# Kernel tuning notes

Measured on AMD Instinct MI355X. Metric: run time of the kernel, lower is better.

Reference implementation:

```python
import jax, jax.numpy as jnp
import numpy as np
import math

N_HEADS = 8
EPS = 1e-12


def _ln(x, g, b):
    m = x.mean(-1, keepdims=True)
    v = ((x - m) ** 2).mean(-1, keepdims=True)
    return (x - m) * jax.lax.rsqrt(v + EPS) * g + b


def _ffn(x, w1, b1, w2, b2):
    # torch nn.GELU default = exact erf gelu; dropout is identity in eval
    return jax.nn.gelu(x @ w1 + b1, approximate=False) @ w2 + b2


def _mha(q_in, kv, mask, qw, qb, kw, kb, vw, vb, ow, ob):
    B, S, _ = q_in.shape
    dh = qw.shape[1] // N_HEADS

    def split(x):
        return x.reshape(B, S, N_HEADS, dh).transpose(0, 2, 1, 3)  # (B,H,S,dh)

    q = split(q_in @ qw + qb) / math.sqrt(dh)
    k = split(kv @ kw + kb)
    v = split(kv @ vw + vb)
    scores = jnp.einsum('bhqd,bhkd->bhqk', q, k) + mask[:, None]
    w = jax.nn.softmax(scores, axis=-1)
    ctx = jnp.einsum('bhqk,bhkd->bhqd', w, v)
    ctx = ctx.transpose(0, 2, 1, 3).reshape(B, S, N_HEADS * dh)
    return ctx @ ow + ob


def reference(hidden, lens,
              f_ffn_w1, f_ffn_b1, f_ffn_w2, f_ffn_b2, f_ln_g, f_ln_b,
              f_q_w, f_q_b, f_k_w, f_k_b, f_v_w, f_v_b, f_o_w, f_o_b,
              b_ffn_w1, b_ffn_b1, b_ffn_w2, b_ffn_b2, b_ln_g, b_ln_b,
              b_q_w, b_q_b, b_k_w, b_k_b, b_v_w, b_v_b, b_o_w, b_o_b,
              attn_ln_g, attn_ln_b,
              out_ffn_w1, out_ffn_b1, out_ffn_w2, out_ffn_b2,
              out_ln_g, out_ln_b):
    S, B, D2 = hidden.shape
    H = D2 // 2
    S2 = S - 2
    f = hidden[..., :H]
    bk = hidden[..., H:]
    query = jnp.concatenate([f[:-2], bk[2:]], axis=-1)        # (S2, B, 2H)
    qbf = jnp.swapaxes(query, 0, 1)                            # (B, S2, 2H)

    # vectorized per-sample length-dependent masks (additive, 0 / -inf)
    qi = jnp.arange(S2)[:, None]
    ki = jnp.arange(S2)[None, :]
    Lm = (lens - 2)[:, None, None]
    # forward: rows >= L-2 all zero; valid rows causal (k <= q) inside [0, L-2)
    f_mask = jnp.where((qi >= Lm) | (ki <= qi), 0.0, -np.inf).astype(hidden.dtype)
    # backward: rows >= L-2 all zero; valid rows anti-causal (k >= q) with k < L-2
    b_mask = jnp.where((qi >= Lm) | ((ki >= qi) & (ki < Lm)), 0.0, -np.inf).astype(hidden.dtype)

    f_q = _ln(_ffn(qbf, f_ffn_w1, f_ffn_b1, f_ffn_w2, f_ffn_b2), f_ln_g, f_ln_b)
    f_kv = jnp.swapaxes(f[:-2], 0, 1)
    f_attn = _mha(f_q, f_kv, f_mask, f_q_w, f_q_b, f_k_w, f_k_b, f_v_w, f_v_b, f_o_w, f_o_b)

    b_q = _ln(_ffn(qbf, b_ffn_w1, b_ffn_b1, b_ffn_w2, b_ffn_b2), b_ln_g, b_ln_b)
    b_kv = jnp.swapaxes(bk[2:], 0, 1)
    b_attn = _mha(b_q, b_kv, b_mask, b_q_w, b_q_b, b_k_w, b_k_b, b_v_w, b_v_b, b_o_w, b_o_b)

    attn_out = _ln(qbf + jnp.concatenate([f_attn, b_attn], axis=-1), attn_ln_g, attn_ln_b)
    out = _ln(_ffn(attn_out, out_ffn_w1, out_ffn_b1, out_ffn_w2, out_ffn_b2), out_ln_g, out_ln_b)
    return jnp.swapaxes(out, 0, 1)                             # (S2, B, 2H)


def setup_inputs():
    key = jax.random.key(0)
    ks = jax.random.split(key, 16)
    S, B, H = 1024, 8, 512
    d = {}
    d['hidden'] = jax.random.normal(ks[0], (S, B, 2 * H), jnp.float32)
    d['lens'] = jax.random.randint(ks[1], (B,), 4, S + 1)

    def w(k, i, o):
        return jax.random.normal(k, (i, o), jnp.float32) * 0.02

    idx = 2
    for p in ('f', 'b'):
        d[p + '_ffn_w1'] = w(ks[idx], 2 * H, 2 * H); idx += 1
        d[p + '_ffn_b1'] = jnp.zeros((2 * H,), jnp.float32)
        d[p + '_ffn_w2'] = w(ks[idx], 2 * H, H); idx += 1
        d[p + '_ffn_b2'] = jnp.zeros((H,), jnp.float32)
        d[p + '_ln_g'] = jnp.ones((H,), jnp.float32)
        d[p + '_ln_b'] = jnp.zeros((H,), jnp.float32)
        for n in ('q', 'k', 'v', 'o'):
            d[p + '_' + n + '_w'] = w(jax.random.fold_in(ks[idx], hash(n) % 97), H, H)
            d[p + '_' + n + '_b'] = jnp.zeros((H,), jnp.float32)
        idx += 1
    d['attn_ln_g'] = jnp.ones((2 * H,), jnp.float32)
    d['attn_ln_b'] = jnp.zeros((2 * H,), jnp.float32)
    d['out_ffn_w1'] = w(ks[idx], 2 * H, 2 * H); idx += 1
    d['out_ffn_b1'] = jnp.zeros((2 * H,), jnp.float32)
    d['out_ffn_w2'] = w(ks[idx], 2 * H, 2 * H); idx += 1
    d['out_ffn_b2'] = jnp.zeros((2 * H,), jnp.float32)
    d['out_ln_g'] = jnp.ones((2 * H,), jnp.float32)
    d['out_ln_b'] = jnp.zeros((2 * H,), jnp.float32)
    return d
```

## Files before the change

kernel.cpp:

```cpp
#include <hip/hip_runtime.h>
#include <cmath>

#define S_ 1024
#define B_ 8
#define H_ 512
#define S2_ 1022
#define M_ (B_*S2_)
#define PAD_ 8192
#define VTS_ ((size_t)8*8*64*1024)

typedef __attribute__((ext_vector_type(8))) short bf16x8;
typedef __attribute__((ext_vector_type(4))) float f32x4;
typedef __attribute__((ext_vector_type(4))) unsigned int u32x4;
typedef __attribute__((ext_vector_type(2))) unsigned int u32x2;

__device__ __forceinline__ unsigned short f2bf(float f){
  unsigned int u = __float_as_uint(f);
  return (unsigned short)((u + 0x7fffu + ((u>>16)&1u)) >> 16);
}
__device__ __forceinline__ float bf2f(unsigned short u){
  return __uint_as_float((unsigned int)u << 16);
}
__device__ __forceinline__ float fgelu(float x){
  float u = x * (0.7978845608f + 0.0356774081f * x * x);
// ... 153 lines not shown
          else {
            int sr = row % S2_, bb2 = row / S2_;
            ((float*)Cout)[((size_t)sr * B_ + bb2) * ldc + col0 + f*16] = v;
          }
        }
      }
    }
  }
}

__global__ __launch_bounds__(512, 2) void lma_gemm8(
    const unsigned short* __restrict__ A, int lda,
    const unsigned short* __restrict__ Bt0, const unsigned short* __restrict__ Bt1,
    const float* __restrict__ bias0, const float* __restrict__ bias1,
    unsigned short* __restrict__ Cout, int ldc,
    int M, int N, int K, int mode, int amap, int nmt)
{
  __shared__ unsigned short Ls[2][2][256*64];
  const int tid = threadIdx.x;
  const int w = tid >> 6, lane = tid & 63, quad = lane >> 4, l16 = lane & 15;
  const int mt = blockIdx.x % nmt, nt = blockIdx.x / nmt;
  const int m0 = mt * 256, n0 = nt * 256;
  const int brch = m0 >> 13;
  const unsigned short* Bt = brch ? Bt1 : Bt0;
  const float* bias = brch ? bias1 : bias0;
  const int coloff = (amap == 2 && brch) ? 512 : 0;
  const int wm = (w >> 2) * 128, wn = (w & 3) * 64;

  f32x4 acc[8][4];
  #pragma unroll
  for (int i = 0; i < 8; i++)
    #pragma unroll
    for (int f = 0; f < 4; f++) acc[i][f] = f32x4{0.f,0.f,0.f,0.f};

  const int lrow8 = lane >> 3;
  const int lkb   = lane & 7;
  const int NT = K >> 6;

  const unsigned short* aP[2][2]; const unsigned short* bP[2][2];
  int aD[2][2], bD[2][2];
  #pragma unroll
  for (int hf = 0; hf < 2; hf++)
    #pragma unroll
    for (int c = 0; c < 2; c++) {
      int rtA = (w>>2)*128 + hf*64 + ((w&3)*2 + c)*8 + lrow8;
      int kbA = lkb ^ (rtA & 7);
      int ga = m0 + rtA;
      int ar;
      if (amap == 0) { ar = (ga > M-1) ? (M-1) : ga; }
      else { ar = ga & (PAD_-1); if (ar > M_-1) ar = M_-1; }
      aP[hf][c] = A + (size_t)ar * lda + coloff + kbA*8;
      aD[hf][c] = ((w>>2)*128 + hf*64 + ((w&3)*2 + c)*8) * 64;
      int rtB = (w>>1)*64 + hf*32 + ((w&1)*2 + c)*8 + lrow8;
      int kbB = lkb ^ (rtB & 7);
      int gb = n0 + rtB; if (gb > N-1) gb = N-1;
      bP[hf][c] = Bt + (size_t)gb * K + kbB*8;
      bD[hf][c] = ((w>>1)*64 + hf*32 + ((w&1)*2 + c)*8) * 64;
    }

  bf16x8 af[4][2], bf[2][2];

  #define STA(buf, hf, kt) { _Pragma("unroll") for (int c = 0; c < 2; c++) \
      glds16(aP[hf][c] + (size_t)(kt)*64, &Ls[buf][0][aD[hf][c]]); }
  #define STB(buf, hf, kt) { _Pragma("unroll") for (int c = 0; c < 2; c++) \
      glds16(bP[hf][c] + (size_t)(kt)*64, &Ls[buf][1][bD[hf][c]]); }
  #define LDA8(buf, mq) { _Pragma("unroll") for (int j = 0; j < 4; j++){ \
      int rt = wm + (mq)*64 + j*16 + l16; \
      const unsigned short* base = &Ls[buf][0][rt*64]; \
      int f_ = rt & 7; \
      af[j][0] = *(const bf16x8*)(base + ((    quad) ^ f_)*8); \
      af[j][1] = *(const bf16x8*)(base + ((4 + quad) ^ f_)*8); } }
  #define LDB8(buf, nq) { _Pragma("unroll") for (int j = 0; j < 2; j++){ \
      int rt = wn + (nq)*32 + j*16 + l16; \
      const unsigned short* base = &Ls[buf][1][rt*64]; \
      int f_ = rt & 7; \
      bf[j][0] = *(const bf16x8*)(base + ((    quad) ^ f_)*8); \
      bf[j][1] = *(const bf16x8*)(base + ((4 + quad) ^ f_)*8); } }
  #define MFMAQ(mq, nq) { __builtin_amdgcn_s_setprio(1); \
      _Pragma("unroll") for (int j = 0; j < 4; j++) \
        _Pragma("unroll") for (int j2 = 0; j2 < 2; j2++){ \
          acc[(mq)*4+j][(nq)*2+j2] = __builtin_amdgcn_mfma_f32_16x16x32_bf16(af[j][0], bf[j2][0], acc[(mq)*4+j][(nq)*2+j2], 0, 0, 0); \
          acc[(mq)*4+j][(nq)*2+j2] = __builtin_amdgcn_mfma_f32_16x16x32_bf16(af[j][1], bf[j2][1], acc[(mq)*4+j][(nq)*2+j2], 0, 0, 0); } \
      __builtin_amdgcn_s_setprio(0); }
  #define BAR()   { SB(); __builtin_amdgcn_s_barrier(); SB(); }
  #define LGKM0() { asm volatile("s_waitcnt lgkmcnt(0)" ::: "memory"); SB(); }
  #define VM6()   { asm volatile("s_waitcnt vmcnt(6)"   ::: "memory"); SB(); }
  #define VM2()   { asm volatile("s_waitcnt vmcnt(2)"   ::: "memory"); SB(); }

  STA(0, 0, 0); STB(0, 0, 0); STB(0, 1, 0); STA(0, 1, 0);
  STA(1, 0, 1);
  asm volatile("s_waitcnt vmcnt(2)" ::: "memory"); SB();
  BAR();

  const int NI = NT >> 1;
  for (int i = 0; i < NI; i++) {
    const int tb  = 2*i + 1;
    int ta2 = 2*i + 2; if (ta2 > NT-1) ta2 = NT-1;
    int tb2 = 2*i + 3; if (tb2 > NT-1) tb2 = NT-1;

    LDA8(0, 0); LDB8(0, 0); STB(1, 0, tb);
    BAR(); LGKM0(); MFMAQ(0, 0); BAR();
    LDB8(0, 1); STB(1, 1, tb);
    BAR(); LGKM0(); MFMAQ(0, 1); BAR();
    LDA8(0, 1); STA(1, 1, tb);
    BAR(); LGKM0(); MFMAQ(1, 1); BAR();
    LDB8(0, 0); STA(0, 0, ta2);
    BAR(); LGKM0(); MFMAQ(1, 0); VM6(); BAR();
    LDA8(1, 0); LDB8(1, 0); STB(0, 1, ta2);
    BAR(); LGKM0(); MFMAQ(0, 0); VM6(); BAR();
    LDB8(1, 1); STA(0, 1, ta2);
    BAR(); LGKM0(); MFMAQ(0, 1); VM6(); BAR();
    LDA8(1, 1); STB(0, 0, ta2);
    BAR(); LGKM0(); MFMAQ(1, 1); BAR();
    LDB8(1, 0); STA(1, 0, tb2);
    BAR(); LGKM0(); MFMAQ(1, 0); VM2(); BAR();
  }
  asm volatile("s_waitcnt vmcnt(0)" ::: "memory");

  float bv[4];
  #pragma unroll
  for (int f = 0; f < 4; f++) bv[f] = bias ? bias[n0 + wn + f*16 + l16] : 0.f;
  const int col0 = n0 + wn + l16;
  #pragma unroll
  for (int i2 = 0; i2 < 8; i2++) {
    #pragma unroll
    for (int r = 0; r < 4; r++) {
      int row = m0 + wm + i2*16 + quad*4 + r;
      if (row < M) {
        #pragma unroll
        for (int f = 0; f < 4; f++) {
          float v = acc[i2][f][r] + bv[f];
          if (mode == 2) v = fgelu(v);
          Cout[(size_t)row * ldc + col0 + f*16] = f2bf(v);
        }
      }
    }
  }
  #undef STA
  #undef STB
  #undef LDA8
  #undef LDB8
  #undef MFMAQ
  #undef BAR
  #undef LGKM0
  #undef VM6
  #undef VM2
}

__global__ __launch_bounds__(512, 2) void lma_gemm8w(
    const unsigned short* __restrict__ A, int lda,
    const unsigned short* __restrict__ Bt0, const unsigned short* __restrict__ Bt1,
    const float* __restrict__ bias0, const float* __restrict__ bias1,
    void* __restrict__ Cout, int ldc,
    int M, int N, int K, int mode, int nmt)
{
  __shared__ unsigned short LsA[2][128*64];
  __shared__ unsigned short LsB[2][256*64];
  const int tid = threadIdx.x;
  const int w = tid >> 6, lane = tid & 63, quad = lane >> 4, l16 = lane & 15;
  const int mt = blockIdx.x % nmt, nt = blockIdx.x / nmt;
  const int m0 = mt * 128, n0 = nt * 256;
  const int brch = m0 >> 13;
  const unsigned short* Bt = brch ? Bt1 : Bt0;
  const float* bias = brch ? bias1 : bias0;
  const int wm = (w >> 2) * 64, wn = (w & 3) * 64;

  f32x4 acc[4][4];
  #pragma unroll
  for (int i = 0; i < 4; i++)
    #pragma unroll
    for (int f = 0; f < 4; f++) acc[i][f] = f32x4{0.f,0.f,0.f,0.f};

  const int lrow8 = lane >> 3;
  const int lkb   = lane & 7;
  const int NT = K >> 6;

  const unsigned short* aP[2]; int aD[2];
  const unsigned short* bP[2][2]; int bD[2][2];
  #pragma unroll
  for (int hf = 0; hf < 2; hf++) {
    int rtA = hf*64 + w*8 + lrow8;
    int kbA = lkb ^ (rtA & 7);
    int ga = m0 + rtA; if (ga > M-1) ga = M-1;
    aP[hf] = A + (size_t)ga * lda + kbA*8;
    aD[hf] = (hf*64 + w*8) * 64;
    #pragma unroll
    for (int c = 0; c < 2; c++) {
      int rtB = hf*128 + (w*2 + c)*8 + lrow8;
      int kbB = lkb ^ (rtB & 7);
      int gb = n0 + rtB; if (gb > N-1) gb = N-1;
      bP[hf][c] = Bt + (size_t)gb * K + kbB*8;
      bD[hf][c] = (hf*128 + (w*2 + c)*8) * 64;
    }
  }

  bf16x8 af[2][2], bf[2][2];

  #define WSTA(buf, hf, kt) { glds16(aP[hf] + (size_t)(kt)*64, &LsA[buf][aD[hf]]); }
  #define WSTB(buf, hf, kt) { _Pragma("unroll") for (int c = 0; c < 2; c++) \
      glds16(bP[hf][c] + (size_t)(kt)*64, &LsB[buf][bD[hf][c]]); }
  #define WLDA(buf, mq) { _Pragma("unroll") for (int j = 0; j < 2; j++){ \
      int rt = wm + (mq)*32 + j*16 + l16; \
      const unsigned short* base = &LsA[buf][rt*64]; \
      int f_ = rt & 7; \
      af[j][0] = *(const bf16x8*)(base + ((    quad) ^ f_)*8); \
      af[j][1] = *(const bf16x8*)(base + ((4 + quad) ^ f_)*8); } }
  #define WLDB(buf, nq) { _Pragma("unroll") for (int j = 0; j < 2; j++){ \
      int rt = wn + (nq)*32 + j*16 + l16; \
      const unsigned short* base = &LsB[buf][rt*64]; \
      int f_ = rt & 7; \
      bf[j][0] = *(const bf16x8*)(base + ((    quad) ^ f_)*8); \
      bf[j][1] = *(const bf16x8*)(base + ((4 + quad) ^ f_)*8); } }
  #define WMFMAQ(mq, nq) { __builtin_amdgcn_s_setprio(1); \
      _Pragma("unroll") for (int j = 0; j < 2; j++) \
        _Pragma("unroll") for (int j2 = 0; j2 < 2; j2++){ \
          acc[(mq)*2+j][(nq)*2+j2] = __builtin_amdgcn_mfma_f32_16x16x32_bf16(af[j][0], bf[j2][0], acc[(mq)*2+j][(nq)*2+j2], 0, 0, 0); \
          acc[(mq)*2+j][(nq)*2+j2] = __builtin_amdgcn_mfma_f32_16x16x32_bf16(af[j][1], bf[j2][1], acc[(mq)*2+j][(nq)*2+j2], 0, 0, 0); } \
      __builtin_amdgcn_s_setprio(0); }
  #define WBAR()   { SB(); __builtin_amdgcn_s_barrier(); SB(); }
  #define WLGKM0() { asm volatile("s_waitcnt lgkmcnt(0)" ::: "memory"); SB(); }
  #define WVM4()   { asm volatile("s_waitcnt vmcnt(4)"   ::: "memory"); SB(); }
  #define WVM1()   { asm volatile("s_waitcnt vmcnt(1)"   ::: "memory"); SB(); }

  WSTA(0, 0, 0); WSTB(0, 0, 0); WSTB(0, 1, 0); WSTA(0, 1, 0);
  WSTA(1, 0, 1);
  WVM1(); WBAR();

  const int NI = NT >> 1;
  for (int i = 0; i < NI; i++) {
    const int tb  = 2*i + 1;
    int ta2 = 2*i + 2; if (ta2 > NT-1) ta2 = NT-1;
    int tb2 = 2*i + 3; if (tb2 > NT-1) tb2 = NT-1;

    WLDA(0, 0); WLDB(0, 0); WSTB(1, 0, tb);
    WBAR(); WLGKM0(); WMFMAQ(0, 0); WBAR();
    WLDB(0, 1); WSTB(1, 1, tb);
    WBAR(); WLGKM0(); WMFMAQ(0, 1); WBAR();
    WLDA(0, 1); WSTA(1, 1, tb);
    WBAR(); WLGKM0(); WMFMAQ(1, 1); WBAR();
    WLDB(0, 0); WSTA(0, 0, ta2);
    WBAR(); WLGKM0(); WMFMAQ(1, 0); WVM4(); WBAR();
    WLDA(1, 0); WLDB(1, 0); WSTB(0, 1, ta2);
    WBAR(); WLGKM0(); WMFMAQ(0, 0); WVM4(); WBAR();
    WLDB(1, 1); WSTA(0, 1, ta2);
    WBAR(); WLGKM0(); WMFMAQ(0, 1); WVM4(); WBAR();
    WLDA(1, 1); WSTB(0, 0, ta2);
    WBAR(); WLGKM0(); WMFMAQ(1, 1); WBAR();
    WLDB(1, 0); WSTA(1, 0, tb2);
    WBAR(); WLGKM0(); WMFMAQ(1, 0); WVM1(); WBAR();
  }
  asm volatile("s_waitcnt vmcnt(0)" ::: "memory");

  float bv[4];
  #pragma unroll
  for (int f = 0; f < 4; f++) bv[f] = bias ? bias[n0 + wn + f*16 + l16] : 0.f;
  const int col0 = n0 + wn + l16;
  #pragma unroll
  for (int i2 = 0; i2 < 4; i2++) {
    #pragma unroll
    for (int r = 0; r < 4; r++) {
      int row = m0 + wm + i2*16 + quad*4 + r;
      if (row < M) {
        #pragma unroll
        for (int f = 0; f < 4; f++) {
          float v = acc[i2][f][r] + bv[f];
          if (mode == 2) v = fgelu(v);
          else if (mode == 1) v *= 0.18033688011112042f;
          if (mode <= 2) ((unsigned short*)Cout)[(size_t)row * ldc + col0 + f*16] = f2bf(v);
          else if (mode == 3) ((float*)Cout)[(size_t)row * ldc + col0 + f*16] = v;
          else {
            int sr = row % S2_, bb2 = row / S2_;
            ((float*)Cout)[((size_t)sr * B_ + bb2) * ldc + col0 + f*16] = v;
          }
        }
      }
    }
  }
  #undef WSTA
  #undef WSTB
  #undef WLDA
  #undef WLDB
  #undef WMFMAQ
  #undef WBAR
  #undef WLGKM0
  #undef WVM4
  #undef WVM1
}

__device__ __forceinline__ void lma_red2(float& s, float& sq){
  __shared__ float red[16];
  #pragma unroll
  for (int msk = 1; msk < 64; msk <<= 1){ s += __shfl_xor(s, msk); sq += __shfl_xor(sq, msk); }
  int w = threadIdx.x >> 6;
  if ((threadIdx.x & 63) == 0){ red[w] = s; red[8 + w] = sq; }
  __syncthreads();
  s  = red[0] + red[1] + red[2] + red[3];
  sq = red[8] + red[9] + red[10] + red[11];
}

__global__ __launch_bounds__(256) void lma_ln(const float* __restrict__ in,
                                              const float* __restrict__ g, const float* __restrict__ bb,
                                              int D, unsigned short* __restrict__ obf, float* __restrict__ of32){
  int row = blockIdx.x, t = threadIdx.x;
  const float* x = in + (size_t)row * D;
  float s = 0.f, sq = 0.f;
  for (int d = t; d < D; d += 256){ float v = x[d]; s += v; sq += v * v; }
  lma_red2(s, sq);
  float mean = s / D;
  float var = sq / D - mean * mean;
  float rstd = rsqrtf(fmaxf(var, 0.f) + 1e-12f);
  if (obf) {
    for (int d = t; d < D; d += 256) obf[(size_t)row * D + d] = f2bf((x[d] - mean) * rstd * g[d] + bb[d]);
  } else {
    for (int d = t; d < D; d += 256) of32[(size_t)row * D + d] = (x[d] - mean) * rstd * g[d] + bb[d];
  }
}

__global__ __launch_bounds__(256) void lma_ln2(const unsigned short* __restrict__ T12b,
                                               const float* __restrict__ fg, const float* __restrict__ fbb,
                                               const float* __restrict__ bg, const float* __restrict__ bbb,
                                               unsigned short* __restrict__ LQ2){
  int m = blockIdx.x, t = threadIdx.x;
  int fb = (m >= M_);
  int idx = m - fb * M_;
  const float* g = fb ? bg : fg;
  const float* bb = fb ? bbb : fbb;
  const unsigned short* x = T12b + ((size_t)fb * PAD_ + idx) * 512;
  unsigned short* o = LQ2 + ((size_t)fb * PAD_ + idx) * 512;
  float v0 = bf2f(x[t]), v1 = bf2f(x[t + 256]);
  float s = v0 + v1, sq = v0*v0 + v1*v1;
  lma_red2(s, sq);
  float mean = s / 512.f;
  float var = sq / 512.f - mean * mean;
  float rstd = rsqrtf(fmaxf(var, 0.f) + 1e-12f);
  o[t]       = f2bf((v0 - mean) * rstd * g[t]       + bb[t]);
  o[t + 256] = f2bf((v1 - mean) * rstd * g[t + 256] + bb[t + 256]);
}

__global__ __launch_bounds__(256) void lma_attn_ln(const unsigned short* __restrict__ pf,
                                                   const unsigned short* __restrict__ pb,
                                                   const float* __restrict__ hidden,
                                                   const float* __restrict__ g, const float* __restrict__ bb,
                                                   unsigned short* __restrict__ out){
  int m = blockIdx.x, t = threadIdx.x;
  int b = m / S2_, s = m - b * S2_;
  const float* hf = hidden + ((size_t)s       * B_ + b) * 1024;
  const float* hb = hidden + ((size_t)(s + 2) * B_ + b) * 1024;
  float v[4]; float sum = 0.f, sq = 0.f;
  #pragma unroll
  for (int j = 0; j < 4; j++){
    int d = t + j * 256;
    float x = (d < 512) ? (bf2f(pf[(size_t)m * 512 + d]) + hf[d])
                        : (bf2f(pb[(size_t)m * 512 + (d - 512)]) + hb[d]);
    v[j] = x; sum += x; sq += x * x;
  }
  lma_red2(sum, sq);
  float mean = sum / 1024.f;
  float var = sq / 1024.f - mean * mean;
  float rstd = rsqrtf(fmaxf(var, 0.f) + 1e-12f);
  #pragma unroll
  for (int j = 0; j < 4; j++){
    int d = t + j * 256;
    out[(size_t)m * 1024 + d] = f2bf((v[j] - mean) * rstd * g[d] + bb[d]);
  }
}

__global__ __launch_bounds__(256, 4) void lma_attn10(const unsigned short* __restrict__ Q2,
                                                     const unsigned short* __restrict__ KV2,
                                                     const unsigned short* __restrict__ VT2,
                                                     unsigned short* __restrict__ CT2,
                                                     const int* __restrict__ lens){
  __shared__ unsigned short Kl[64*64];
  __shared__ unsigned short Vl[64*64];
  __shared__ __align__(16) unsigned short Pl[4][16*64];

  const int tid = threadIdx.x;
  const int w = tid >> 6, lane = tid & 63, quad = lane >> 4, l16 = lane & 15;
  const int id = blockIdx.x;
  const int qt = id >> 6, h = (id >> 3) & 7, b = id & 7;
  const int L2 = lens[b] - 2;
  const int q0wg = qt * 64;
  const int q0 = q0wg + w * 16;
  const int qg = q0 + l16;
  const int qload = (qg > S2_-1) ? (S2_-1) : qg;

  const size_t qbase  = ((size_t)b * S2_) * 512  + h * 64;
  const size_t kbase  = ((size_t)b * S2_) * 1024 + h * 64;
  const size_t vtbase = ((size_t)(b * 8 + h) * 64) * 1024;
  char* Pb = (char*)&Pl[w][0];

  const int lrow = lane >> 3;
  const int g0s  = (lane & 7) ^ lrow;
  const int x7   = l16 & 7;
  const int x7s  = x7 << 4;

  for (int fb = 0; fb < 2; fb++) {
    const int backward = fb;
    const unsigned short* Q  = Q2  + (size_t)fb * PAD_ * 512;
    const unsigned short* Kx = KV2 + (size_t)fb * PAD_ * 1024;
    const unsigned short* VT = VT2 + (size_t)fb * VTS_;
    unsigned short* CTX      = CT2 + (size_t)fb * PAD_ * 512;

    bf16x8 qf[2];
    {
      const unsigned short* qp = Q + qbase + (size_t)qload * 512 + quad * 8;
      qf[0] = *(const bf16x8*)(qp);
      qf[1] = *(const bf16x8*)(qp + 32);
    }

    float mi = -3e38f, li = 0.f;
    f32x4 ot[4];
    #pragma unroll
    for (int f = 0; f < 4; f++) ot[f] = f32x4{0.f,0.f,0.f,0.f};

    int klo = 0, khi = S2_ - 1;
    if (q0wg + 63 < L2) {
      if (!backward) khi = q0wg + 63;
      else { klo = q0wg; khi = L2 - 1; }
    }

    for (int kt0 = klo; kt0 <= khi; kt0 += 64) {
      #pragma unroll
      for (int c = 0; c < 2; c++) {
        int r = w*16 + c*8 + lrow;
        int kr = kt0 + r; if (kr > S2_-1) kr = S2_-1;
        glds16(Kx + kbase + (size_t)kr * 1024 + g0s * 8, &Kl[(w*16 + c*8) * 64]);
        glds16(VT + vtbase + (size_t)r * 1024 + kt0 + g0s * 8, &Vl[(w*16 + c*8) * 64]);
      }
      __syncthreads();

      bf16x8 kf[4][2], vf[4][2];
      #pragma unroll
      for (int sub = 0; sub < 4; sub++) {
        const unsigned short* kp = &Kl[(sub*16 + l16) * 64];
        kf[sub][0] = *(const bf16x8*)(kp + (( quad      ^ x7) * 8));
        kf[sub][1] = *(const bf16x8*)(kp + (((quad + 4) ^ x7) * 8));
      }
      #pragma unroll
      for (int f = 0; f < 4; f++) {
        const unsigned short* vp = &Vl[(f*16 + l16) * 64];
        vf[f][0] = *(const bf16x8*)(vp + (( quad      ^ x7) * 8));
        vf[f][1] = *(const bf16x8*)(vp + (((quad + 4) ^ x7) * 8));
      }

      f32x4 st[4];
      __builtin_amdgcn_s_setprio(1);
      #pragma unroll
      for (int sub = 0; sub < 4; sub++) {
        f32x4 s = f32x4{0.f,0.f,0.f,0.f};
        s = __builtin_amdgcn_mfma_f32_16x16x32_bf16(kf[sub][0], qf[0], s, 0, 0, 0);
        s = __builtin_amdgcn_mfma_f32_16x16x32_bf16(kf[sub][1], qf[1], s, 0, 0, 0);
        st[sub] = s;
      }
      __builtin_amdgcn_s_setprio(0);

      {
        bool tail = (kt0 + 63 > S2_ - 1);
        bool full;
        if (!backward) full = !tail && ((kt0 + 63 <= q0) || (q0 >= L2));
        else           full = !tail && ((q0 >= L2) || ((kt0 >= q0 + 15) && (kt0 + 63 < L2)));
        if (!full) {
          #pragma unroll
          for (int sub = 0; sub < 4; sub++) {
            #pragma unroll
            for (int r = 0; r < 4; r++) {
              int kg = kt0 + sub*16 + quad*4 + r;
              bool ok;
              if (!backward) ok = (kg < S2_) && ((qg >= L2) || (kg <= qg));
              else           ok = (kg < S2_) && ((qg >= L2) || ((kg >= qg) && (kg < L2)));
              if (!ok) st[sub][r] = -3e38f;
            }
          }
        }
      }

      float mx = -3e38f;
      #pragma unroll
      for (int sub = 0; sub < 4; sub++)
        #pragma unroll
        for (int r = 0; r < 4; r++) mx = fmaxf(mx, st[sub][r]);
      mx = fmaxf(mx, __shfl_xor(mx, 16));
      mx = fmaxf(mx, __shfl_xor(mx, 32));

      if (__any(mx > mi + 11.f)) {
        float mn = fmaxf(mi, mx);
        float al = fexp2(mi - mn);
        li *= al;
        #pragma unroll
        for (int f = 0; f < 4; f++)
          #pragma unroll
          for (int r = 0; r < 4; r++) ot[f][r] *= al;
        mi = mn;
      }

      float rs = 0.f;
      #pragma unroll
      for (int sub = 0; sub < 4; sub++)
        #pragma unroll
        for (int r = 0; r < 4; r++) {
          float p = fexp2(st[sub][r] - mi);
          st[sub][r] = p; rs += p;
        }
      rs += __shfl_xor(rs, 16);
      rs += __shfl_xor(rs, 32);
      li += rs;

      #pragma unroll
      for (int sub = 0; sub < 4; sub++) {
        u32x2 pk2;
        pk2[0] = cvtpk(st[sub][0], st[sub][1]);
        pk2[1] = cvtpk(st[sub][2], st[sub][3]);
        *(u32x2*)(Pb + (l16*128 + ((sub*32 + quad*8) ^ x7s))) = pk2;
      }
      bf16x8 pfr0 = *(const bf16x8*)(Pb + (l16*128 + (( 0 + quad*16) ^ x7s)));
      bf16x8 pfr1 = *(const bf16x8*)(Pb + (l16*128 + ((64 + quad*16) ^ x7s)));

      __builtin_amdgcn_s_setprio(1);
      #pragma unroll
      for (int f = 0; f < 4; f++) {
        ot[f] = __builtin_amdgcn_mfma_f32_16x16x32_bf16(vf[f][0], pfr0, ot[f], 0, 0, 0);
        ot[f] = __builtin_amdgcn_mfma_f32_16x16x32_bf16(vf[f][1], pfr1, ot[f], 0, 0, 0);
      }
      __builtin_amdgcn_s_setprio(0);
      __syncthreads();
    }

    if (qg < S2_) {
      float rcp = 1.f / li;
      #pragma unroll
      for (int f = 0; f < 4; f++) {
        ushort4 pk;
        pk.x = f2bf(ot[f][0] * rcp); pk.y = f2bf(ot[f][1] * rcp);
        pk.z = f2bf(ot[f][2] * rcp); pk.w = f2bf(ot[f][3] * rcp);
        *(ushort4*)&CTX[qbase + (size_t)qg * 512 + f*16 + quad*4] = pk;
      }
    }
  }
}

extern "C" void kernel_launch(void* const* d_in, const int* in_sizes, int n_in,
                              void* d_out, int out_size, void* d_ws, size_t ws_size,
                              hipStream_t stream)
{
  const float* hidden = (const float*)d_in[0];
  const int*   lens   = (const int*)d_in[1];
  const float* fw[14]; for (int i = 0; i < 14; i++) fw[i] = (const float*)d_in[2 + i];
  const float* bw[14]; for (int i = 0; i < 14; i++) bw[i] = (const float*)d_in[16 + i];
  const float* attn_g = (const float*)d_in[30];
  const float* attn_b = (const float*)d_in[31];
  const float* o_w1 = (const float*)d_in[32];
  const float* o_b1 = (const float*)d_in[33];
  const float* o_w2 = (const float*)d_in[34];
  const float* o_b2 = (const float*)d_in[35];
  const float* o_lng = (const float*)d_in[36];
  const float* o_lnb = (const float*)d_in[37];

  char* ws = (char*)d_ws;
  size_t off = 0;
  auto alloc = [&](size_t bytes)->char* {
    off = (off + 255) & ~(size_t)255;
    char* p = ws + off; off += bytes; return p;
  };

  unsigned short* fw1t = (unsigned short*)alloc((size_t)1024*1024*2);
  unsigned short* fw2t = (unsigned short*)alloc((size_t)512*1024*2);
  unsigned short* fqt  = (unsigned short*)alloc((size_t)512*512*2);
  unsigned short* fkvt = (unsigned short*)alloc((size_t)1024*512*2);
  unsigned short* fot  = (unsigned short*)alloc((size_t)512*512*2);
  unsigned short* bw1t = (unsigned short*)alloc((size_t)1024*1024*2);
  unsigned short* bw2t = (unsigned short*)alloc((size_t)512*1024*2);
  unsigned short* bqt  = (unsigned short*)alloc((size_t)512*512*2);
  unsigned short* bkvt = (unsigned short*)alloc((size_t)1024*512*2);
  unsigned short* bot  = (unsigned short*)alloc((size_t)512*512*2);
  unsigned short* ow1t = (unsigned short*)alloc((size_t)1024*1024*2);
  unsigned short* ow2t = (unsigned short*)alloc((size_t)1024*1024*2);
  float*          biasKV = (float*)alloc(2048*4);

  unsigned short* Xb   = (unsigned short*)alloc((size_t)M_*1024*2);
  unsigned short* big1 = (unsigned short*)alloc((size_t)2*PAD_*1024*2);
  float*          big2 = (float*)alloc((size_t)2*PAD_*512*4);
  unsigned short* LQCT = (unsigned short*)alloc((size_t)2*PAD_*512*2);
  unsigned short* Q2   = (unsigned short*)alloc((size_t)2*PAD_*512*2);

  unsigned short* H12 = big1, *KV2 = big1, *H1o = big1;
  unsigned short* T12b = (unsigned short*)big2;
  unsigned short* VT2  = (unsigned short*)big2;
  unsigned short* P2b  = (unsigned short*)big2 + 2*VTS_;
  unsigned short* LQ2 = LQCT, *CT2 = LQCT;

  lma_prep_x<<<M_, 256, 0, stream>>>(hidden, Xb);

  {
    TPack tp;
    const float* srcs[14] = { fw[0], fw[2], fw[6], fw[8], fw[10], fw[12],
                              bw[0], bw[2], bw[6], bw[8], bw[10], bw[12],
                              o_w1, o_w2 };
    unsigned short* dsts[14] = { fw1t, fw2t, fqt, fkvt, fkvt + (size_t)512*512, fot,
                                 bw1t, bw2t, bqt, bkvt, bkvt + (size_t)512*512, bot,
                                 ow1t, ow2t };
    int Ks[14] = {1024,1024,512,512,512,512, 1024,1024,512,512,512,512, 1024,1024};
    int Ns[14] = {1024, 512,512,512,512,512, 1024, 512,512,512,512,512, 1024,1024};
    for (int i = 0; i < 14; i++){ tp.src[i]=srcs[i]; tp.dst[i]=dsts[i]; tp.K[i]=Ks[i]; tp.N[i]=Ns[i]; }
    lma_transpose_all<<<dim3(32, 32, 14), 256, 0, stream>>>(tp);
  }
  lma_biascat<<<8, 256, 0, stream>>>(fw[9], fw[11], bw[9], bw[11], biasKV);

  auto G8 = [&](const unsigned short* A, int lda,
                const unsigned short* B0, const unsigned short* B1,
                const float* b0, const float* b1,
                unsigned short* C, int ldc, int M, int N, int K, int mode, int amap){
    int nmt = M / 256;
    lma_gemm8<<<dim3(nmt * (N/256)), 512, 0, stream>>>(A, lda, B0, B1, b0, b1, C, ldc, M, N, K, mode, amap, nmt);
  };
  auto G8W = [&](const unsigned short* A, int lda,
                 const unsigned short* B0, const unsigned short* B1,
                 const float* b0, const float* b1,
                 void* C, int ldc, int M, int N, int K, int mode){
    int nmt = (M + 127) / 128;
    lma_gemm8w<<<dim3(nmt * (N/256)), 512, 0, stream>>>(A, lda, B0, B1, b0, b1, C, ldc, M, N, K, mode, nmt);
  };

  G8(Xb, 1024, fw1t, bw1t, fw[1], bw[1], H12, 1024, 2*PAD_, 1024, 1024, 2, 1);
  G8W(H12, 1024, fw2t, bw2t, fw[3], bw[3], T12b, 512, 2*PAD_, 512, 1024, 0);
  lma_ln2<<<2*M_, 256, 0, stream>>>(T12b, fw[4], fw[5], bw[4], bw[5], LQ2);
  G8W(LQ2, 512, fqt, bqt, fw[7], bw[7], Q2, 512, 2*PAD_, 512, 512, 1);
  G8(Xb, 1024, fkvt, bkvt, biasKV, biasKV + 1024, KV2, 1024, 2*PAD_, 1024, 512, 0, 2);
  lma_vt2<<<dim3(32, 16, 16), 256, 0, stream>>>(KV2, VT2);

  lma_attn10<<<dim3(1024), 256, 0, stream>>>(Q2, KV2, VT2, CT2, lens);

  G8W(CT2, 512, fot, bot, fw[13], bw[13], P2b, 512, 2*PAD_, 512, 512, 0);

  lma_attn_ln<<<M_, 256, 0, stream>>>(P2b, P2b + (size_t)PAD_*512, hidden, attn_g, attn_b, Xb);

  G8W(Xb, 1024, ow1t, ow1t, o_b1, o_b1, H1o, 1024, M_, 1024, 1024, 2);
  G8W(H1o, 1024, ow2t, ow2t, o_b2, o_b2, (float*)d_out, 1024, M_, 1024, 1024, 4);
  lma_ln<<<M_, 256, 0, stream>>>((float*)d_out, o_lng, o_lnb, 1024, nullptr, (float*)d_out);
}
```

Baseline: 550.8 us.

## Process two 64-key tiles per attention loop iteration

The attention kernel now loads two K/V tiles (128 keys) into double-sized shared buffers per iteration. It computes both score blocks and applies a single online-softmax max/rescale over both. This halves the barriers and softmax rescale steps per key and gives more independent loads in flight. In exchange it doubles K/V LDS usage and adds register pressure, which may reduce occupancy.

Measured after the change: 545.4 us. No clear change (-1.0%).

```diff
diff --git a/kernel.cpp b/kernel.cpp
--- a/kernel.cpp
+++ b/kernel.cpp
@@ -542,13 +542,13 @@
   }
 }
 
-__global__ __launch_bounds__(256, 4) void lma_attn10(const unsigned short* __restrict__ Q2,
+__global__ __launch_bounds__(256, 4) void lma_attn11(const unsigned short* __restrict__ Q2,
                                                      const unsigned short* __restrict__ KV2,
                                                      const unsigned short* __restrict__ VT2,
                                                      unsigned short* __restrict__ CT2,
                                                      const int* __restrict__ lens){
-  __shared__ unsigned short Kl[64*64];
-  __shared__ unsigned short Vl[64*64];
+  __shared__ unsigned short Kl[2][64*64];
+  __shared__ unsigned short Vl[2][64*64];
   __shared__ __align__(16) unsigned short Pl[4][16*64];
 
   const int tid = threadIdx.x;
@@ -596,46 +596,71 @@
       else { klo = q0wg; khi = L2 - 1; }
     }
 
-    for (int kt0 = klo; kt0 <= khi; kt0 += 64) {
+    for (int kt0 = klo; kt0 <= khi; kt0 += 128) {
+      const bool h2 = (kt0 + 64 <= khi);
+      const int span = h2 ? 127 : 63;
+
       #pragma unroll
       for (int c = 0; c < 2; c++) {
         int r = w*16 + c*8 + lrow;
         int kr = kt0 + r; if (kr > S2_-1) kr = S2_-1;
-        glds16(Kx + kbase + (size_t)kr * 1024 + g0s * 8, &Kl[(w*16 + c*8) * 64]);
-        glds16(VT + vtbase + (size_t)r * 1024 + kt0 + g0s * 8, &Vl[(w*16 + c*8) * 64]);
+        glds16(Kx + kbase + (size_t)kr * 1024 + g0s * 8, &Kl[0][(w*16 + c*8) * 64]);
+        glds16(VT + vtbase + (size_t)r * 1024 + kt0 + g0s * 8, &Vl[0][(w*16 + c*8) * 64]);
+      }
+      if (h2) {
+        #pragma unroll
+        for (int c = 0; c < 2; c++) {
+          int r = w*16 + c*8 + lrow;
+          int kr = kt0 + 64 + r; if (kr > S2_-1) kr = S2_-1;
+          glds16(Kx + kbase + (size_t)kr * 1024 + g0s * 8, &Kl[1][(w*16 + c*8) * 64]);
+          glds16(VT + vtbase + (size_t)r * 1024 + (kt0 + 64) + g0s * 8, &Vl[1][(w*16 + c*8) * 64]);
+        }
       }
       __syncthreads();
 
-      bf16x8 kf[4][2], vf[4][2];
-      #pragma unroll
-      for (int sub = 0; sub < 4; sub++) {
-        const unsigned short* kp = &Kl[(sub*16 + l16) * 64];
-        kf[sub][0] = *(const bf16x8*)(kp + (( quad      ^ x7) * 8));
-        kf[sub][1] = *(const bf16x8*)(kp + (((quad + 4) ^ x7) * 8));
-      }
-      #pragma unroll
-      for (int f = 0; f < 4; f++) {
-        const unsigned short* vp = &Vl[(f*16 + l16) * 64];
-        vf[f][0] = *(const bf16x8*)(vp + (( quad      ^ x7) * 8));
-        vf[f][1] = *(const bf16x8*)(vp + (((quad + 4) ^ x7) * 8));
-      }
-
-      f32x4 st[4];
-      __builtin_amdgcn_s_setprio(1);
-      #pragma unroll
-      for (int sub = 0; sub < 4; sub++) {
-        f32x4 s = f32x4{0.f,0.f,0.f,0.f};
-        s = __builtin_amdgcn_mfma_f32_16x16x32_bf16(kf[sub][0], qf[0], s, 0, 0, 0);
-        s = __builtin_amdgcn_mfma_f32_16x16x32_bf16(kf[sub][1], qf[1], s, 0, 0, 0);
-        st[sub] = s;
-      }
-      __builtin_amdgcn_s_setprio(0);
-
+      f32x4 st[8];
       {
-        bool tail = (kt0 + 63 > S2_ - 1);
+        bf16x8 kf[4][2];
+        #pragma unroll
+        for (int sub = 0; sub < 4; sub++) {
+          const unsigned short* kp = &Kl[0][(sub*16 + l16) * 64];
+          kf[sub][0] = *(const bf16x8*)(kp + (( quad      ^ x7) * 8));
+          kf[sub][1] = *(const bf16x8*)(kp + (((quad + 4) ^ x7) * 8));
+        }
+        __builtin_amdgcn_s_setprio(1);
+        #pragma unroll
+        for (int sub = 0; sub < 4; sub++) {
+          f32x4 s = f32x4{0.f,0.f,0.f,0.f};
+          s = __builtin_amdgcn_mfma_f32_16x16x32_bf16(kf[sub][0], qf[0], s, 0, 0, 0);
+          s = __builtin_amdgcn_mfma_f32_16x16x32_bf16(kf[sub][1], qf[1], s, 0, 0, 0);
+          st[sub] = s;
+        }
+        __builtin_amdgcn_s_setprio(0);
+      }
+      if (h2) {
+        bf16x8 kf[4][2];
+        #pragma unroll
+        for (int sub = 0; sub < 4; sub++) {
+          const unsigned short* kp = &Kl[1][(sub*16 + l16) * 64];
+          kf[sub][0] = *(const bf16x8*)(kp + (( quad      ^ x7) * 8));
+          kf[sub][1] = *(const bf16x8*)(kp + (((quad + 4) ^ x7) * 8));
+        }
+        __builtin_amdgcn_s_setprio(1);
+        #pragma unroll
+        for (int sub = 0; sub < 4; sub++) {
+          f32x4 s = f32x4{0.f,0.f,0.f,0.f};
+          s = __builtin_amdgcn_mfma_f32_16x16x32_bf16(kf[sub][0], qf[0], s, 0, 0, 0);
+          s = __builtin_amdgcn_mfma_f32_16x16x32_bf16(kf[sub][1], qf[1], s, 0, 0, 0);
+          st[4 + sub] = s;
+        }
+        __builtin_amdgcn_s_setprio(0);
+      }
+
+      {
+        bool tail = (kt0 + span > S2_ - 1);
         bool full;
-        if (!backward) full = !tail && ((kt0 + 63 <= q0) || (q0 >= L2));
-        else           full = !tail && ((q0 >= L2) || ((kt0 >= q0 + 15) && (kt0 + 63 < L2)));
+        if (!backward) full = !tail && ((kt0 + span <= q0) || (q0 >= L2));
+        else           full = !tail && ((q0 >= L2) || ((kt0 >= q0 + 15) && (kt0 + span < L2)));
         if (!full) {
           #pragma unroll
           for (int sub = 0; sub < 4; sub++) {
@@ -648,6 +673,19 @@
               if (!ok) st[sub][r] = -3e38f;
             }
           }
+          if (h2) {
+            #pragma unroll
+            for (int sub = 0; sub < 4; sub++) {
+              #pragma unroll
+              for (int r = 0; r < 4; r++) {
+                int kg = kt0 + 64 + sub*16 + quad*4 + r;
+                bool ok;
+                if (!backward) ok = (kg < S2_) && ((qg >= L2) || (kg <= qg));
+                else           ok = (kg < S2_) && ((qg >= L2) || ((kg >= qg) && (kg < L2)));
+                if (!ok) st[4 + sub][r] = -3e38f;
+              }
+            }
+          }
         }
       }
 
@@ -656,6 +694,12 @@
       for (int sub = 0; sub < 4; sub++)
         #pragma unroll
         for (int r = 0; r < 4; r++) mx = fmaxf(mx, st[sub][r]);
+      if (h2) {
+        #pragma unroll
+        for (int sub = 4; sub < 8; sub++)
+          #pragma unroll
+          for (int r = 0; r < 4; r++) mx = fmaxf(mx, st[sub][r]);
+      }
       mx = fmaxf(mx, __shfl_xor(mx, 16));
       mx = fmaxf(mx, __shfl_xor(mx, 32));
 
@@ -678,6 +722,15 @@
           float p = fexp2(st[sub][r] - mi);
           st[sub][r] = p; rs += p;
         }
+      if (h2) {
+        #pragma unroll
+        for (int sub = 4; sub < 8; sub++)
+          #pragma unroll
+          for (int r = 0; r < 4; r++) {
+            float p = fexp2(st[sub][r] - mi);
+            st[sub][r] = p; rs += p;
+          }
+      }
       rs += __shfl_xor(rs, 16);
       rs += __shfl_xor(rs, 32);
       li += rs;
@@ -689,16 +742,49 @@
         pk2[1] = cvtpk(st[sub][2], st[sub][3]);
         *(u32x2*)(Pb + (l16*128 + ((sub*32 + quad*8) ^ x7s))) = pk2;
       }
-      bf16x8 pfr0 = *(const bf16x8*)(Pb + (l16*128 + (( 0 + quad*16) ^ x7s)));
-      bf16x8 pfr1 = *(const bf16x8*)(Pb + (l16*128 + ((64 + quad*16) ^ x7s)));
-
-      __builtin_amdgcn_s_setprio(1);
-      #pragma unroll
-      for (int f = 0; f < 4; f++) {
-        ot[f] = __builtin_amdgcn_mfma_f32_16x16x32_bf16(vf[f][0], pfr0, ot[f], 0, 0, 0);
-        ot[f] = __builtin_amdgcn_mfma_f32_16x16x32_bf16(vf[f][1], pfr1, ot[f], 0, 0, 0);
-      }
-      __builtin_amdgcn_s_setprio(0);
+      {
+        bf16x8 pfr0 = *(const bf16x8*)(Pb + (l16*128 + (( 0 + quad*16) ^ x7s)));
+        bf16x8 pfr1 = *(const bf16x8*)(Pb + (l16*128 + ((64 + quad*16) ^ x7s)));
+        bf16x8 vf[4][2];
+        #pragma unroll
+        for (int f = 0; f < 4; f++) {
+          const unsigned short* vp = &Vl[0][(f*16 + l16) * 64];
+          vf[f][0] = *(const bf16x8*)(vp + (( quad      ^ x7) * 8));
+          vf[f][1] = *(const bf16x8*)(vp + (((quad + 4) ^ x7) * 8));
+        }
+        __builtin_amdgcn_s_setprio(1);
+        #pragma unroll
+        for (int f = 0; f < 4; f++) {
+          ot[f] = __builtin_amdgcn_mfma_f32_16x16x32_bf16(vf[f][0], pfr0, ot[f], 0, 0, 0);
+          ot[f] = __builtin_amdgcn_mfma_f32_16x16x32_bf16(vf[f][1], pfr1, ot[f], 0, 0, 0);
+        }
+        __builtin_amdgcn_s_setprio(0);
+      }
+      if (h2) {
+        #pragma unroll
+        for (int sub = 0; sub < 4; sub++) {
+          u32x2 pk2;
+          pk2[0] = cvtpk(st[4+sub][0], st[4+sub][1]);
+          pk2[1] = cvtpk(st[4+sub][2], st[4+sub][3]);
+          *(u32x2*)(Pb + (l16*128 + ((sub*32 + quad*8) ^ x7s))) = pk2;
+        }
+        bf16x8 pfr0 = *(const bf16x8*)(Pb + (l16*128 + (( 0 + quad*16) ^ x7s)));
+        bf16x8 pfr1 = *(const bf16x8*)(Pb + (l16*128 + ((64 + quad*16) ^ x7s)));
+        bf16x8 vf[4][2];
+        #pragma unroll
+        for (int f = 0; f < 4; f++) {
+          const unsigned short* vp = &Vl[1][(f*16 + l16) * 64];
+          vf[f][0] = *(const bf16x8*)(vp + (( quad      ^ x7) * 8));
+          vf[f][1] = *(const bf16x8*)(vp + (((quad + 4) ^ x7) * 8));
+        }
+        __builtin_amdgcn_s_setprio(1);
+        #pragma unroll
+        for (int f = 0; f < 4; f++) {
+          ot[f] = __builtin_amdgcn_mfma_f32_16x16x32_bf16(vf[f][0], pfr0, ot[f], 0, 0, 0);
+          ot[f] = __builtin_amdgcn_mfma_f32_16x16x32_bf16(vf[f][1], pfr1, ot[f], 0, 0, 0);
+        }
+        __builtin_amdgcn_s_setprio(0);
+      }
       __syncthreads();
     }
 
@@ -804,7 +890,7 @@
   G8(Xb, 1024, fkvt, bkvt, biasKV, biasKV + 1024, KV2, 1024, 2*PAD_, 1024, 512, 0, 2);
   lma_vt2<<<dim3(32, 16, 16), 256, 0, stream>>>(KV2, VT2);
 
-  lma_attn10<<<dim3(1024), 256, 0, stream>>>(Q2, KV2, VT2, CT2, lens);
+  lma_attn11<<<dim3(1024), 256, 0, stream>>>(Q2, KV2, VT2, CT2, lens);
 
   G8W(CT2, 512, fot, bot, fw[13], bw[13], P2b, 512, 2*PAD_, 512, 512, 0);
 
```

## Restructure attention to 128-query tiles with fwd/bwd split across blocks

Applied to the files above, without the earlier changes.

The attention kernel now gives each workgroup 128 queries (two 16-row sub-tiles per wave) instead of 64, so each K/V tile loaded into shared memory is reused twice as much. The forward and backward directions move from a loop inside the block onto separate blocks, which keeps the grid at 1024 blocks. Separately, the GEMM barrier and vmcnt macros drop their scheduling barriers, which gives the compiler more freedom to reorder. The costs are higher register pressure from doubled accumulators and a coarser causal skip range per block.

New measurement: 577.2 us. +4.8%, slower.

```diff
diff --git a/kernel.cpp b/kernel.cpp
--- a/kernel.cpp
+++ b/kernel.cpp
@@ -259,14 +259,14 @@
           acc[(mq)*4+j][(nq)*2+j2] = __builtin_amdgcn_mfma_f32_16x16x32_bf16(af[j][0], bf[j2][0], acc[(mq)*4+j][(nq)*2+j2], 0, 0, 0); \
           acc[(mq)*4+j][(nq)*2+j2] = __builtin_amdgcn_mfma_f32_16x16x32_bf16(af[j][1], bf[j2][1], acc[(mq)*4+j][(nq)*2+j2], 0, 0, 0); } \
       __builtin_amdgcn_s_setprio(0); }
-  #define BAR()   { SB(); __builtin_amdgcn_s_barrier(); SB(); }
+  #define BAR()   { __builtin_amdgcn_s_barrier(); }
   #define LGKM0() { asm volatile("s_waitcnt lgkmcnt(0)" ::: "memory"); SB(); }
-  #define VM6()   { asm volatile("s_waitcnt vmcnt(6)"   ::: "memory"); SB(); }
-  #define VM2()   { asm volatile("s_waitcnt vmcnt(2)"   ::: "memory"); SB(); }
+  #define VM6()   { asm volatile("s_waitcnt vmcnt(6)"   ::: "memory"); }
+  #define VM2()   { asm volatile("s_waitcnt vmcnt(2)"   ::: "memory"); }
 
   STA(0, 0, 0); STB(0, 0, 0); STB(0, 1, 0); STA(0, 1, 0);
   STA(1, 0, 1);
-  asm volatile("s_waitcnt vmcnt(2)" ::: "memory"); SB();
+  asm volatile("s_waitcnt vmcnt(2)" ::: "memory");
   BAR();
 
   const int NI = NT >> 1;
@@ -394,10 +394,10 @@
           acc[(mq)*2+j][(nq)*2+j2] = __builtin_amdgcn_mfma_f32_16x16x32_bf16(af[j][0], bf[j2][0], acc[(mq)*2+j][(nq)*2+j2], 0, 0, 0); \
           acc[(mq)*2+j][(nq)*2+j2] = __builtin_amdgcn_mfma_f32_16x16x32_bf16(af[j][1], bf[j2][1], acc[(mq)*2+j][(nq)*2+j2], 0, 0, 0); } \
       __builtin_amdgcn_s_setprio(0); }
-  #define WBAR()   { SB(); __builtin_amdgcn_s_barrier(); SB(); }
+  #define WBAR()   { __builtin_amdgcn_s_barrier(); }
   #define WLGKM0() { asm volatile("s_waitcnt lgkmcnt(0)" ::: "memory"); SB(); }
-  #define WVM4()   { asm volatile("s_waitcnt vmcnt(4)"   ::: "memory"); SB(); }
-  #define WVM1()   { asm volatile("s_waitcnt vmcnt(1)"   ::: "memory"); SB(); }
+  #define WVM4()   { asm volatile("s_waitcnt vmcnt(4)"   ::: "memory"); }
+  #define WVM1()   { asm volatile("s_waitcnt vmcnt(1)"   ::: "memory"); }
 
   WSTA(0, 0, 0); WSTB(0, 0, 0); WSTB(0, 1, 0); WSTA(0, 1, 0);
   WSTA(1, 0, 1);
@@ -542,24 +542,30 @@
   }
 }
 
-__global__ __launch_bounds__(256, 4) void lma_attn10(const unsigned short* __restrict__ Q2,
+__global__ __launch_bounds__(256, 4) void lma_attn12(const unsigned short* __restrict__ Q2,
                                                      const unsigned short* __restrict__ KV2,
                                                      const unsigned short* __restrict__ VT2,
                                                      unsigned short* __restrict__ CT2,
                                                      const int* __restrict__ lens){
   __shared__ unsigned short Kl[64*64];
   __shared__ unsigned short Vl[64*64];
-  __shared__ __align__(16) unsigned short Pl[4][16*64];
+  __shared__ __align__(16) unsigned short Pl[4][2*16*64];
 
   const int tid = threadIdx.x;
   const int w = tid >> 6, lane = tid & 63, quad = lane >> 4, l16 = lane & 15;
   const int id = blockIdx.x;
-  const int qt = id >> 6, h = (id >> 3) & 7, b = id & 7;
+  const int b = id & 7, h = (id >> 3) & 7, qt = (id >> 6) & 7, fb = id >> 9;
+  const int backward = fb;
   const int L2 = lens[b] - 2;
-  const int q0wg = qt * 64;
-  const int q0 = q0wg + w * 16;
-  const int qg = q0 + l16;
-  const int qload = (qg > S2_-1) ? (S2_-1) : qg;
+  const int q0wg = qt * 128;
+
+  int q0s[2], qgs[2], qls[2];
+  #pragma unroll
+  for (int s = 0; s < 2; s++){
+    q0s[s] = q0wg + (w + 4*s) * 16;
+    qgs[s] = q0s[s] + l16;
+    qls[s] = (qgs[s] > S2_-1) ? (S2_-1) : qgs[s];
+  }
 
   const size_t qbase  = ((size_t)b * S2_) * 512  + h * 64;
   const size_t kbase  = ((size_t)b * S2_) * 1024 + h * 64;
@@ -571,71 +577,71 @@
   const int x7   = l16 & 7;
   const int x7s  = x7 << 4;
 
-  for (int fb = 0; fb < 2; fb++) {
-    const int backward = fb;
-    const unsigned short* Q  = Q2  + (size_t)fb * PAD_ * 512;
-    const unsigned short* Kx = KV2 + (size_t)fb * PAD_ * 1024;
-    const unsigned short* VT = VT2 + (size_t)fb * VTS_;
-    unsigned short* CTX      = CT2 + (size_t)fb * PAD_ * 512;
-
-    bf16x8 qf[2];
+  const unsigned short* Q  = Q2  + (size_t)fb * PAD_ * 512;
+  const unsigned short* Kx = KV2 + (size_t)fb * PAD_ * 1024;
+  const unsigned short* VT = VT2 + (size_t)fb * VTS_;
+  unsigned short* CTX      = CT2 + (size_t)fb * PAD_ * 512;
+
+  bf16x8 qf[2][2];
+  #pragma unroll
+  for (int s = 0; s < 2; s++){
+    const unsigned short* qp = Q + qbase + (size_t)qls[s] * 512 + quad * 8;
+    qf[s][0] = *(const bf16x8*)(qp);
+    qf[s][1] = *(const bf16x8*)(qp + 32);
+  }
+
+  float mi[2] = {-3e38f, -3e38f}, li[2] = {0.f, 0.f};
+  f32x4 ot[2][4];
+  #pragma unroll
+  for (int s = 0; s < 2; s++)
+    #pragma unroll
+    for (int f = 0; f < 4; f++) ot[s][f] = f32x4{0.f,0.f,0.f,0.f};
+
+  int klo = 0, khi = S2_ - 1;
+  if (q0wg + 127 < L2) {
+    if (!backward) khi = q0wg + 127;
+    else { klo = q0wg; khi = L2 - 1; }
+  }
+
+  for (int kt0 = klo; kt0 <= khi; kt0 += 64) {
+    #pragma unroll
+    for (int c = 0; c < 2; c++) {
+      int r = w*16 + c*8 + lrow;
+      int kr = kt0 + r; if (kr > S2_-1) kr = S2_-1;
+      glds16(Kx + kbase + (size_t)kr * 1024 + g0s * 8, &Kl[(w*16 + c*8) * 64]);
+      glds16(VT + vtbase + (size_t)r * 1024 + kt0 + g0s * 8, &Vl[(w*16 + c*8) * 64]);
+    }
+    __syncthreads();
+
+    f32x4 st[2][4];
     {
-      const unsigned short* qp = Q + qbase + (size_t)qload * 512 + quad * 8;
-      qf[0] = *(const bf16x8*)(qp);
-      qf[1] = *(const bf16x8*)(qp + 32);
-    }
-
-    float mi = -3e38f, li = 0.f;
-    f32x4 ot[4];
-    #pragma unroll
-    for (int f = 0; f < 4; f++) ot[f] = f32x4{0.f,0.f,0.f,0.f};
-
-    int klo = 0, khi = S2_ - 1;
-    if (q0wg + 63 < L2) {
-      if (!backward) khi = q0wg + 63;
-      else { klo = q0wg; khi = L2 - 1; }
-    }
-
-    for (int kt0 = klo; kt0 <= khi; kt0 += 64) {
-      #pragma unroll
-      for (int c = 0; c < 2; c++) {
-        int r = w*16 + c*8 + lrow;
-        int kr = kt0 + r; if (kr > S2_-1) kr = S2_-1;
-        glds16(Kx + kbase + (size_t)kr * 1024 + g0s * 8, &Kl[(w*16 + c*8) * 64]);
-        glds16(VT + vtbase + (size_t)r * 1024 + kt0 + g0s * 8, &Vl[(w*16 + c*8) * 64]);
-      }
-      __syncthreads();
-
-      bf16x8 kf[4][2], vf[4][2];
+      bf16x8 kf[4][2];
       #pragma unroll
       for (int sub = 0; sub < 4; sub++) {
         const unsigned short* kp = &Kl[(sub*16 + l16) * 64];
         kf[sub][0] = *(const bf16x8*)(kp + (( quad      ^ x7) * 8));
         kf[sub][1] = *(const bf16x8*)(kp + (((quad + 4) ^ x7) * 8));
       }
-      #pragma unroll
-      for (int f = 0; f < 4; f++) {
-        const unsigned short* vp = &Vl[(f*16 + l16) * 64];
-        vf[f][0] = *(const bf16x8*)(vp + (( quad      ^ x7) * 8));
-        vf[f][1] = *(const bf16x8*)(vp + (((quad + 4) ^ x7) * 8));
-      }
-
-      f32x4 st[4];
       __builtin_amdgcn_s_setprio(1);
       #pragma unroll
-      for (int sub = 0; sub < 4; sub++) {
-        f32x4 s = f32x4{0.f,0.f,0.f,0.f};
-        s = __builtin_amdgcn_mfma_f32_16x16x32_bf16(kf[sub][0], qf[0], s, 0, 0, 0);
-        s = __builtin_amdgcn_mfma_f32_16x16x32_bf16(kf[sub][1], qf[1], s, 0, 0, 0);
-        st[sub] = s;
-      }
+      for (int s = 0; s < 2; s++)
+        #pragma unroll
+        for (int sub = 0; sub < 4; sub++) {
+          f32x4 acc = f32x4{0.f,0.f,0.f,0.f};
+          acc = __builtin_amdgcn_mfma_f32_16x16x32_bf16(kf[sub][0], qf[s][0], acc, 0, 0, 0);
+          acc = __builtin_amdgcn_mfma_f32_16x16x32_bf16(kf[sub][1], qf[s][1], acc, 0, 0, 0);
+          st[s][sub] = acc;
+        }
       __builtin_amdgcn_s_setprio(0);
-
-      {
-        bool tail = (kt0 + 63 > S2_ - 1);
+    }
+
+    {
+      bool tail = (kt0 + 63 > S2_ - 1);
+      #pragma unroll
+      for (int s = 0; s < 2; s++) {
         bool full;
-        if (!backward) full = !tail && ((kt0 + 63 <= q0) || (q0 >= L2));
-        else           full = !tail && ((q0 >= L2) || ((kt0 >= q0 + 15) && (kt0 + 63 < L2)));
+        if (!backward) full = !tail && ((kt0 + 63 <= q0s[s]) || (q0s[s] >= L2));
+        else           full = !tail && ((q0s[s] >= L2) || ((kt0 >= q0s[s] + 15) && (kt0 + 63 < L2)));
         if (!full) {
           #pragma unroll
           for (int sub = 0; sub < 4; sub++) {
@@ -643,73 +649,93 @@
             for (int r = 0; r < 4; r++) {
               int kg = kt0 + sub*16 + quad*4 + r;
               bool ok;
-              if (!backward) ok = (kg < S2_) && ((qg >= L2) || (kg <= qg));
-              else           ok = (kg < S2_) && ((qg >= L2) || ((kg >= qg) && (kg < L2)));
-              if (!ok) st[sub][r] = -3e38f;
+              if (!backward) ok = (kg < S2_) && ((qgs[s] >= L2) || (kg <= qgs[s]));
+              else           ok = (kg < S2_) && ((qgs[s] >= L2) || ((kg >= qgs[s]) && (kg < L2)));
+              if (!ok) st[s][sub][r] = -3e38f;
             }
           }
         }
       }
-
+    }
+
+    #pragma unroll
+    for (int s = 0; s < 2; s++) {
       float mx = -3e38f;
       #pragma unroll
       for (int sub = 0; sub < 4; sub++)
         #pragma unroll
-        for (int r = 0; r < 4; r++) mx = fmaxf(mx, st[sub][r]);
+        for (int r = 0; r < 4; r++) mx = fmaxf(mx, st[s][sub][r]);
       mx = fmaxf(mx, __shfl_xor(mx, 16));
       mx = fmaxf(mx, __shfl_xor(mx, 32));
-
-      if (__any(mx > mi + 11.f)) {
-        float mn = fmaxf(mi, mx);
-        float al = fexp2(mi - mn);
-        li *= al;
+      if (__any(mx > mi[s] + 11.f)) {
+        float mn = fmaxf(mi[s], mx);
+        float al = fexp2(mi[s] - mn);
+        li[s] *= al;
         #pragma unroll
         for (int f = 0; f < 4; f++)
           #pragma unroll
-          for (int r = 0; r < 4; r++) ot[f][r] *= al;
-        mi = mn;
-      }
-
+          for (int r = 0; r < 4; r++) ot[s][f][r] *= al;
+        mi[s] = mn;
+      }
       float rs = 0.f;
       #pragma unroll
       for (int sub = 0; sub < 4; sub++)
         #pragma unroll
         for (int r = 0; r < 4; r++) {
-          float p = fexp2(st[sub][r] - mi);
-          st[sub][r] = p; rs += p;
+          float p = fexp2(st[s][sub][r] - mi[s]);
+          st[s][sub][r] = p; rs += p;
         }
       rs += __shfl_xor(rs, 16);
       rs += __shfl_xor(rs, 32);
-      li += rs;
-
+      li[s] += rs;
+    }
+
+    #pragma unroll
+    for (int s = 0; s < 2; s++) {
+      char* Pbs = Pb + s * 2048;
       #pragma unroll
       for (int sub = 0; sub < 4; sub++) {
         u32x2 pk2;
-        pk2[0] = cvtpk(st[sub][0], st[sub][1]);
-        pk2[1] = cvtpk(st[sub][2], st[sub][3]);
-        *(u32x2*)(Pb + (l16*128 + ((sub*32 + quad*8) ^ x7s))) = pk2;
-      }
-      bf16x8 pfr0 = *(const bf16x8*)(Pb + (l16*128 + (( 0 + quad*16) ^ x7s)));
-      bf16x8 pfr1 = *(const bf16x8*)(Pb + (l16*128 + ((64 + quad*16) ^ x7s)));
-
-      __builtin_amdgcn_s_setprio(1);
+        pk2[0] = cvtpk(st[s][sub][0], st[s][sub][1]);
+        pk2[1] = cvtpk(st[s][sub][2], st[s][sub][3]);
+        *(u32x2*)(Pbs + (l16*128 + ((sub*32 + quad*8) ^ x7s))) = pk2;
+      }
+    }
+    {
+      bf16x8 vf[4][2];
       #pragma unroll
       for (int f = 0; f < 4; f++) {
-        ot[f] = __builtin_amdgcn_mfma_f32_16x16x32_bf16(vf[f][0], pfr0, ot[f], 0, 0, 0);
-        ot[f] = __builtin_amdgcn_mfma_f32_16x16x32_bf16(vf[f][1], pfr1, ot[f], 0, 0, 0);
-      }
-      __builtin_amdgcn_s_setprio(0);
-      __syncthreads();
-    }
-
-    if (qg < S2_) {
-      float rcp = 1.f / li;
+        const unsigned short* vp = &Vl[(f*16 + l16) * 64];
+        vf[f][0] = *(const bf16x8*)(vp + (( quad      ^ x7) * 8));
+        vf[f][1] = *(const bf16x8*)(vp + (((quad + 4) ^ x7) * 8));
+      }
+      #pragma unroll
+      for (int s = 0; s < 2; s++) {
+        char* Pbs = Pb + s * 2048;
+        bf16x8 pfr0 = *(const bf16x8*)(Pbs + (l16*128 + (( 0 + quad*16) ^ x7s)));
+        bf16x8 pfr1 = *(const bf16x8*)(Pbs + (l16*128 + ((64 + quad*16) ^ x7s)));
+        __builtin_amdgcn_s_setprio(1);
+        #pragma unroll
+        for (int f = 0; f < 4; f++) {
+          ot[s][f] = __builtin_amdgcn_mfma_f32_16x16x32_bf16(vf[f][0], pfr0, ot[s][f], 0, 0, 0);
+          ot[s][f] = __builtin_amdgcn_mfma_f32_16x16x32_bf16(vf[f][1], pfr1, ot[s][f], 0, 0, 0);
+        }
+        __builtin_amdgcn_s_setprio(0);
+      }
+    }
+    __syncthreads();
+  }
+
+  #pragma unroll
+  for (int s = 0; s < 2; s++) {
+    if (qgs[s] < S2_) {
+      float rcp = 1.f / li[s];
       #pragma unroll
       for (int f = 0; f < 4; f++) {
         ushort4 pk;
-        pk.x = f2bf(ot[f][0] * rcp); pk.y = f2bf(ot[f][1] * rcp);
-        pk.z = f2bf(ot[f][2] * rcp); pk.w = f2bf(ot[f][3] * rcp);
-        *(ushort4*)&CTX[qbase + (size_t)qg * 512 + f*16 + quad*4] = pk;
+        pk.x = f2bf(ot[s][f][0] * rcp); pk.y = f2bf(ot[s][f][1] * rcp);
+        pk.z = f2bf(ot[s][f][2] * rcp); pk.w = f2bf(ot[s][f][3] * rcp);
+        *(ushort4*)&CTX[qbase + (size_t)qgs[s] * 512 + f*16 + quad*4] = pk;
       }
     }
   }
@@ -804,7 +830,7 @@
   G8(Xb, 1024, fkvt, bkvt, biasKV, biasKV + 1024, KV2, 1024, 2*PAD_, 1024, 512, 0, 2);
   lma_vt2<<<dim3(32, 16, 16), 256, 0, stream>>>(KV2, VT2);
 
-  lma_attn10<<<dim3(1024), 256, 0, stream>>>(Q2, KV2, VT2, CT2, lens);
+  lma_attn12<<<dim3(1024), 256, 0, stream>>>(Q2, KV2, VT2, CT2, lens);
 
   G8W(CT2, 512, fot, bot, fw[13], bw[13], P2b, 512, 2*PAD_, 512, 512, 0);
 
```
